# Optimization experiments

Measured on AMD Instinct MI355X. Metric: run time of the kernel, lower is better.

Reference implementation:

```python
import jax, jax.numpy as jnp
import numpy as np

B = 8192
DV, DT = 1024, 768          # visual / text dims
H = 256                     # hidden_dim
C = 5                       # num_classes
GH = 128                    # gate_hidden_dim
K = 8                       # graph_k
ALPHA = 0.5                 # graph_alpha
EW = 0.01                   # entropy_weight
FD = 2 * H                  # fused_dim = 512
GI = FD + C + H             # gate input dim = 773
NEG = -1.0e9
LN_EPS = 1e-5
BN_EPS = 1e-5
N_IMAGES = 512


def setup_inputs() -> dict:
    key = jax.random.key(0)
    ks = jax.random.split(key, 20)
    def rn(k, sh, s=0.02):
        return jax.random.normal(k, sh, dtype=jnp.float32) * s
    # x = [visual(1024) | text(768) | bbox_ctx(4) | img_uid(1)]
    xf = jax.random.normal(ks[0], (B, DV + DT), dtype=jnp.float32)
    bbox = jax.random.uniform(ks[1], (B, 4), dtype=jnp.float32)
    img = jax.random.randint(ks[2], (B, 1), 0, N_IMAGES).astype(jnp.float32)
    x = jnp.concatenate([xf, bbox, img], axis=1)  # [B, 1797]
    return {
        "x": x,
        "ln_v_g": jnp.ones((DV,), jnp.float32), "ln_v_b": jnp.zeros((DV,), jnp.float32),
        "ln_t_g": jnp.ones((DT,), jnp.float32), "ln_t_b": jnp.zeros((DT,), jnp.float32),
        "W_v": rn(ks[3], (DV, H)), "b_v": jnp.zeros((H,), jnp.float32),
        "W_t": rn(ks[4], (DT, H)), "b_t": jnp.zeros((H,), jnp.float32),
        "W_cp": rn(ks[5], (FD, C)), "b_cp": jnp.zeros((C,), jnp.float32),
        "W_ctx1": rn(ks[6], (FD, H)), "b_ctx1": jnp.zeros((H,), jnp.float32),
        "W_ctx2": rn(ks[7], (H, H)), "b_ctx2": jnp.zeros((H,), jnp.float32),
        "W_g1": rn(ks[8], (GI, GH)), "b_g1": jnp.zeros((GH,), jnp.float32),
        "W_g2": rn(ks[9], (GH, 2)), "b_g2": jnp.zeros((2,), jnp.float32),
        "W_gu1": rn(ks[10], (FD, FD)), "b_gu1": jnp.zeros((FD,), jnp.float32),
        "W_gu2": rn(ks[11], (FD, FD)), "b_gu2": jnp.zeros((FD,), jnp.float32),
        "W_c1": rn(ks[12], (FD, H)), "b_c1": jnp.zeros((H,), jnp.float32),
        "bn_g": jnp.ones((H,), jnp.float32), "bn_b": jnp.zeros((H,), jnp.float32),
        "W_c2": rn(ks[13], (H, C)), "b_c2": jnp.zeros((C,), jnp.float32),
    }


def _layernorm(x, g, b):
    m = jnp.mean(x, axis=-1, keepdims=True)
    v = jnp.mean((x - m) ** 2, axis=-1, keepdims=True)
    return (x - m) * jax.lax.rsqrt(v + LN_EPS) * g + b


def _knn_aggregate(features, coords, img):
    """KNN over 2D spatial coords with same-image masking; softmax-weighted gather."""
    n = features.shape[0]
    sq = jnp.sum(coords * coords, axis=1)
    d2 = sq[:, None] + sq[None, :] - 2.0 * (coords @ coords.T)
    sim = -jnp.sqrt(jnp.clip(d2, 0.0))                 # [B, B] = -cdist
    eye = jnp.eye(n, dtype=bool)
    same = (img[None, :] == img[:, None]) & ~eye
    has_neighbor = jnp.any(same, axis=1)
    sim_same = jnp.where(same, sim, NEG)
    sim = jnp.where(has_neighbor[:, None], sim_same, sim)
    sim = jnp.where(eye, NEG, sim)
    vals, idx = jax.lax.top_k(sim, K)                  # [B, K]
    w = jax.nn.softmax(vals, axis=1)
    return jnp.einsum('bk,bkd->bd', w, features[idx])  # gather + weighted sum


def reference(x, ln_v_g, ln_v_b, ln_t_g, ln_t_b, W_v, b_v, W_t, b_t,
              W_cp, b_cp, W_ctx1, b_ctx1, W_ctx2, b_ctx2,
              W_g1, b_g1, W_g2, b_g2, W_gu1, b_gu1, W_gu2, b_gu2,
              W_c1, b_c1, bn_g, bn_b, W_c2, b_c2):
    xv = x[:, 0:DV]
    xt = x[:, DV:DV + DT]
    coords = x[:, DV + DT:DV + DT + 2]     # bbox_ctx[:, :2]
    img = x[:, DV + DT + 4]                # img_uid[:, 0]

    fv = _layernorm(xv, ln_v_g, ln_v_b) @ W_v + b_v
    ft = _layernorm(xt, ln_t_g, ln_t_b) @ W_t + b_t
    base_fused = jnp.concatenate([fv, ft], axis=1)     # [B, FD]

    class_prior = jax.lax.stop_gradient(jax.nn.softmax(base_fused @ W_cp + b_cp, axis=1))

    neigh_agg = _knn_aggregate(base_fused, coords, img)
    spatial_token = jax.nn.relu(neigh_agg @ W_ctx1 + b_ctx1) @ W_ctx2 + b_ctx2
    spatial_token = jax.lax.stop_gradient(spatial_token)

    gate_in = jnp.concatenate([base_fused, class_prior, spatial_token], axis=1)
    gate_logits = jax.nn.relu(gate_in @ W_g1 + b_g1) @ W_g2 + b_g2
    gate_probs = jax.nn.softmax(gate_logits / 1.0, axis=1)  # temperature=1.0 (eval: dropout off)
    entropy = -jnp.sum(gate_probs * jnp.log(gate_probs + 1e-8), axis=1)
    entropy_loss = jnp.mean(entropy) * EW

    fused = jnp.concatenate([fv * gate_probs[:, 0:1], ft * gate_probs[:, 1:2]], axis=1)
    spatial_update = _knn_aggregate(fused, coords, img)
    upd = jax.nn.relu(spatial_update @ W_gu1 + b_gu1) @ W_gu2 + b_gu2
    fused = fused + ALPHA * upd

    h = fused @ W_c1 + b_c1
    # eval-mode BatchNorm1d: running_mean=0, running_var=1
    h = h * (bn_g / jnp.sqrt(1.0 + BN_EPS)) + bn_b
    h = jax.nn.relu(h)
    logits = h @ W_c2 + b_c2
    return logits, entropy_loss
```

## Files before the change

### kernel.cpp

```cpp
#include <hip/hip_runtime.h>
#include <math.h>

#define B_ROWS 8192
#define DV_DIM 1024
#define DT_DIM 768
#define H_DIM 256
#define C_CLS 5
#define GH_DIM 128
#define K_NN 8
#define FD_DIM 512
#define GIP_DIM 832
#define GI_REAL 773
#define XCOLS 1797
#define NEGV -1000000000.0f
#define LN_EPS_F 1e-5f
#define BN_EPS_F 1e-5f
#define N_IMG 512
#define EW_F 0.01f
#define ALPHA_F 0.5f

typedef __attribute__((ext_vector_type(8))) short short8v;
typedef __attribute__((ext_vector_type(4))) float f32x4;

__device__ inline short bf16r(float f) {
    unsigned u = __float_as_uint(f);
    return (short)((u + 0x7fffu + ((u >> 16) & 1u)) >> 16);
}

__device__ inline float bf2f(short s) {
    return __uint_as_float(((unsigned)(unsigned short)s) << 16);
}

struct PrepArgs {
    const float* W[8];
    short* h[8];
    int K[8];
    int N[8];
    int Kpad[8];
    int cnt[8];
};

__global__ void prep_all_kernel(PrepArgs a, const float* __restrict__ x,
                                float* __restrict__ cx, float* __restrict__ cy,
                                float* __restrict__ sq, int* __restrict__ imgi,
                                int* __restrict__ cnt) {
    int idx = blockIdx.x * blockDim.x + threadIdx.x;
#pragma unroll
    for (int s = 0; s < 8; ++s) {
        if (idx < a.cnt[s]) {
            int Kp = a.Kpad[s];
            int n = idx / Kp, k = idx - n * Kp;
            float f = (k < a.K[s]) ? a.W[s][(size_t)k * a.N[s] + n] : 0.f;
            a.h[s][idx] = bf16r(f);
            return;
        }
        idx -= a.cnt[s];
    }
    if (idx < B_ROWS) {
        const float* row = x + (size_t)idx * XCOLS;
        float av = row[DV_DIM + DT_DIM];
        float bv = row[DV_DIM + DT_DIM + 1];
        cx[idx] = av; cy[idx] = bv; sq[idx] = av * av + bv * bv;
        int m = (int)row[DV_DIM + DT_DIM + 4];
        imgi[idx] = m;
        atomicAdd(&cnt[m], 1);
    }
}

__global__ void scan_kernel(const int* __restrict__ cnt, int* __restrict__ start,
                            int* __restrict__ cursor) {
    __shared__ int s[N_IMG];
    int t = threadIdx.x;
    s[t] = cnt[t];
    __syncthreads();
    for (int off = 1; off < N_IMG; off <<= 1) {
        int v = (t >= off) ? s[t - off] : 0;
        __syncthreads();
        s[t] += v;
        __syncthreads();
    }
    int st = s[t] - cnt[t];
    start[t] = st;
    cursor[t] = st;
}

__global__ void scatter_kernel(const int* __restrict__ imgi, int* __restrict__ cursor,
                               int* __restrict__ perm) {
    int i = blockIdx.x * blockDim.x + threadIdx.x;
    if (i >= B_ROWS) return;
    int pos = atomicAdd(&cursor[imgi[i]], 1);
    perm[pos] = i;
}

#define KNN_BLOCKS 32
#define LN_BLOCKS (B_ROWS / 4)
__global__ __launch_bounds__(256) void lnknn_kernel(
    const float* __restrict__ x,
    const float* __restrict__ gv, const float* __restrict__ bv,
    const float* __restrict__ gt, const float* __restrict__ bt,
    short* __restrict__ xvh, short* __restrict__ xth,
    const float* __restrict__ cx, const float* __restrict__ cy,
    const float* __restrict__ sq, const int* __restrict__ imgi,
    const int* __restrict__ cnt, const int* __restrict__ start,
    const int* __restrict__ perm, int* __restrict__ knn_idx,
    float* __restrict__ knn_w) {
    if (blockIdx.x < KNN_BLOCKS) {
        int i = blockIdx.x * 256 + threadIdx.x;
        if (i >= B_ROWS) return;
        float xi = cx[i], yi = cy[i], si = sq[i];
        float vals[K_NN];
        int ids[K_NN];
#pragma unroll
        for (int k = 0; k < K_NN; ++k) { vals[k] = NEGV; ids[k] = i; }
        int m = imgi[i];
        int s = cnt[m];
        if (s >= 2) {
            int st = start[m];
            for (int t = 0; t < s; ++t) {
                int j = perm[st + t];
                if (j == i) continue;
                float d2 = si + sq[j] - 2.f * (xi * cx[j] + yi * cy[j]);
                d2 = fmaxf(d2, 0.f);
                float v = -sqrtf(d2);
                if (v > vals[K_NN - 1]) {
                    int p = K_NN - 1;
                    while (p > 0 && vals[p - 1] < v) {
                        vals[p] = vals[p - 1]; ids[p] = ids[p - 1]; --p;
                    }
                    vals[p] = v; ids[p] = j;
                }
            }
        } else {
            for (int j = 0; j < B_ROWS; ++j) {
                if (j == i) continue;
                float d2 = si + sq[j] - 2.f * (xi * cx[j] + yi * cy[j]);
                d2 = fmaxf(d2, 0.f);
                float v = -sqrtf(d2);
                if (v > vals[K_NN - 1]) {
                    int p = K_NN - 1;
                    while (p > 0 && vals[p - 1] < v) {
                        vals[p] = vals[p - 1]; ids[p] = ids[p - 1]; --p;
                    }
                    vals[p] = v; ids[p] = j;
                }
            }
        }
        float mx = vals[0];
        float e[K_NN];
        float sum = 0.f;
#pragma unroll
        for (int k = 0; k < K_NN; ++k) { e[k] = expf(vals[k] - mx); sum += e[k]; }
        float inv = 1.f / sum;
#pragma unroll
        for (int k = 0; k < K_NN; ++k) {
            knn_w[(size_t)i * K_NN + k] = e[k] * inv;
            knn_idx[(size_t)i * K_NN + k] = ids[k];
        }
        return;
    }
    int wave = threadIdx.x >> 6;
    int lane = threadIdx.x & 63;
    long row = (long)(blockIdx.x - KNN_BLOCKS) * 4 + wave;
    const float* xr = x + row * XCOLS;

    float v[16];
#pragma unroll
    for (int k = 0; k < 16; ++k) v[k] = xr[lane + 64 * k];
    float sum = 0.f;
#pragma unroll
    for (int k = 0; k < 16; ++k) sum += v[k];
#pragma unroll
    for (int off = 32; off; off >>= 1) sum += __shfl_xor(sum, off);
    float mean = sum * (1.f / DV_DIM);
    float vs = 0.f;
#pragma unroll
    for (int k = 0; k < 16; ++k) { float d = v[k] - mean; vs += d * d; }
#pragma unroll
    for (int off = 32; off; off >>= 1) vs += __shfl_xor(vs, off);
    float rs = rsqrtf(vs * (1.f / DV_DIM) + LN_EPS_F);
#pragma unroll
    for (int k = 0; k < 16; ++k) {
        int j = lane + 64 * k;
        float y = (v[k] - mean) * rs * gv[j] + bv[j];
        xvh[row * DV_DIM + j] = bf16r(y);
    }

    float u[12];
#pragma unroll
    for (int k = 0; k < 12; ++k) u[k] = xr[DV_DIM + lane + 64 * k];
    sum = 0.f;
#pragma unroll
    for (int k = 0; k < 12; ++k) sum += u[k];
#pragma unroll
    for (int off = 32; off; off >>= 1) sum += __shfl_xor(sum, off);
    mean = sum * (1.f / DT_DIM);
    vs = 0.f;
#pragma unroll
    for (int k = 0; k < 12; ++k) { float d = u[k] - mean; vs += d * d; }
#pragma unroll
    for (int off = 32; off; off >>= 1) vs += __shfl_xor(vs, off);
    rs = rsqrtf(vs * (1.f / DT_DIM) + LN_EPS_F);
#pragma unroll
    for (int k = 0; k < 12; ++k) {
        int j = lane + 64 * k;
        float y = (u[k] - mean) * rs * gt[j] + bt[j];
        xth[row * DT_DIM + j] = bf16r(y);
    }
}

__device__ inline int xcd_swz(int wg, int nwg) {
    int q = nwg >> 3, r = nwg & 7;
    int xc = wg & 7, ii = wg >> 3;
    return (xc < r ? xc * (q + 1) : r * (q + 1) + (xc - r) * q) + ii;
}

struct GemmPair {
    const short* Ah;
    const short* Bh;
    const float* bias;
    int K; int ncb; int colOff;
};

template <int MODE, int NF>
__global__ __launch_bounds__(256) void gemm2_kernel(
    GemmPair P0, GemmPair P1, int nblk0,
    short* __restrict__ Ch, int ldc,
    const short* __restrict__ auxh, const float* __restrict__ gpv) {
    constexpr int ASZ = 4096;
    constexpr int BSZ = 32 * NF * 64;
    __shared__ short lds[ASZ + BSZ];
    short* sAh = lds;
    short* sBh = lds + ASZ;

    const int tid = threadIdx.x;
    const int lane = tid & 63;
    const int wave = tid >> 6;
    const int wm = wave >> 1, wn = wave & 1;
    const int l15 = lane & 15, lq = lane >> 4;

    int wid = xcd_swz(blockIdx.x, gridDim.x);
    GemmPair G = P0;
    if (wid >= nblk0) { G = P1; wid -= nblk0; }

    const int panel = wid / G.ncb, cb = wid - panel * G.ncb;
    const long rowBase = (long)panel * 64;
    const int colBase = cb * (32 * NF);
    const int K = G.K;

    f32x4 acc[2][NF];
#pragma unroll
    for (int i = 0; i < 2; ++i)
#pragma unroll
        for (int j = 0; j < NF; ++j) acc[i][j] = (f32x4){0.f, 0.f, 0.f, 0.f};

    short8v pAh[2], pBh[NF];
    const int ar0 = tid >> 3, ac = tid & 7;
    const int ar1 = (tid + 256) >> 3;

    {
        long go0 = (rowBase + ar0) * K + ac * 8;
        long go1 = (rowBase + ar1) * K + ac * 8;
        pAh[0] = *(const short8v*)(G.Ah + go0);
        pAh[1] = *(const short8v*)(G.Ah + go1);
#pragma unroll
        for (int j = 0; j < NF; ++j) {
            int cid = tid + 256 * j;
            int cl = cid >> 3, c = cid & 7;
            long go = (colBase + cl) * (long)K + c * 8;
            pBh[j] = *(const short8v*)(G.Bh + go);
        }
    }

    const int nsteps = K >> 6;
    for (int s = 0; s < nsteps; ++s) {
        __syncthreads();
        {
            int off0 = ar0 * 64 + ((ac ^ (ar0 & 7)) << 3);
            int off1 = ar1 * 64 + ((ac ^ (ar1 & 7)) << 3);
            *(short8v*)(sAh + off0) = pAh[0];
            *(short8v*)(sAh + off1) = pAh[1];
#pragma unroll
            for (int j = 0; j < NF; ++j) {
                int cid = tid + 256 * j;
                int cl = cid >> 3, c = cid & 7;
                int off = cl * 64 + ((c ^ (cl & 7)) << 3);
                *(short8v*)(sBh + off) = pBh[j];
            }
        }
        __syncthreads();
        if (s + 1 < nsteps) {
            long ko = (long)(s + 1) * 64;
            long go0 = (rowBase + ar0) * K + ko + ac * 8;
            long go1 = (rowBase + ar1) * K + ko + ac * 8;
            pAh[0] = *(const short8v*)(G.Ah + go0);
            pAh[1] = *(const short8v*)(G.Ah + go1);
#pragma unroll
            for (int j = 0; j < NF; ++j) {
                int cid = tid + 256 * j;
                int cl = cid >> 3, c = cid & 7;
                long go = (colBase + cl) * (long)K + ko + c * 8;
                pBh[j] = *(const short8v*)(G.Bh + go);
            }
        }
#pragma unroll
        for (int ksub = 0; ksub < 2; ++ksub) {
            int cc = ksub * 4 + lq;
            short8v afh[2], bfh[NF];
#pragma unroll
            for (int mf = 0; mf < 2; ++mf) {
                int rr = wm * 32 + mf * 16 + l15;
                int off = rr * 64 + ((cc ^ (rr & 7)) << 3);
                afh[mf] = *(short8v*)(sAh + off);
            }
#pragma unroll
            for (int nf = 0; nf < NF; ++nf) {
                int cl = wn * (NF * 16) + nf * 16 + l15;
                int off = cl * 64 + ((cc ^ (cl & 7)) << 3);
                bfh[nf] = *(short8v*)(sBh + off);
            }
#pragma unroll
            for (int mf = 0; mf < 2; ++mf)
#pragma unroll
                for (int nf = 0; nf < NF; ++nf)
                    acc[mf][nf] = __builtin_amdgcn_mfma_f32_16x16x32_bf16(afh[mf], bfh[nf], acc[mf][nf], 0, 0, 0);
        }
    }

#pragma unroll
    for (int mf = 0; mf < 2; ++mf)
#pragma unroll
        for (int nf = 0; nf < NF; ++nf) {
            int col = colBase + wn * (NF * 16) + nf * 16 + l15;
            long row0 = rowBase + wm * 32 + mf * 16 + lq * 4;
#pragma unroll
            for (int rr = 0; rr < 4; ++rr) {
                long row = row0 + rr;
                float v = acc[mf][nf][rr] + G.bias[col];
                long o = row * ldc + G.colOff + col;
                if (MODE == 4) {
                    Ch[o] = bf16r(v);
                } else if (MODE == 3) {
                    Ch[o] = bf16r(fmaxf(v, 0.f));
                } else {
                    float g = gpv[row * 2 + (col >= H_DIM ? 1 : 0)];
                    float fv = bf2f(auxh[row * FD_DIM + col]) * g + ALPHA_F * v;
                    Ch[o] = bf16r(fv);
                }
            }
        }
}

__global__ __launch_bounds__(256) void post_base_kernel(
    const short* __restrict__ baseh, const float* __restrict__ Wcp,
    const float* __restrict__ bcp, const int* __restrict__ kidx,
    const float* __restrict__ wgt, short* __restrict__ gih,
    short* __restrict__ aggh) {
    int row = blockIdx.x;
    int t = threadIdx.x;
    short sa = baseh[(size_t)row * FD_DIM + t];
    short sb = baseh[(size_t)row * FD_DIM + t + 256];
    float a = bf2f(sa), b = bf2f(sb);

    __shared__ float red[C_CLS][256];
#pragma unroll
    for (int n = 0; n < C_CLS; ++n)
        red[n][t] = a * Wcp[t * C_CLS + n] + b * Wcp[(t + 256) * C_CLS + n];
    __syncthreads();
    for (int off = 128; off; off >>= 1) {
        if (t < off) {
#pragma unroll
            for (int n = 0; n < C_CLS; ++n) red[n][t] += red[n][t + off];
        }
        __syncthreads();
    }
    size_t go = (size_t)row * GIP_DIM;
    if (t == 0) {
        float lg[C_CLS];
#pragma unroll
        for (int n = 0; n < C_CLS; ++n) lg[n] = red[n][0] + bcp[n];
        float mx = lg[0];
#pragma unroll
        for (int n = 1; n < C_CLS; ++n) mx = fmaxf(mx, lg[n]);
        float s = 0.f;
        float e[C_CLS];
#pragma unroll
        for (int n = 0; n < C_CLS; ++n) { e[n] = expf(lg[n] - mx); s += e[n]; }
        float inv = 1.f / s;
#pragma unroll
        for (int n = 0; n < C_CLS; ++n) gih[go + FD_DIM + n] = bf16r(e[n] * inv);
    }
    gih[go + t] = sa;
    gih[go + t + 256] = sb;
    if (t < GIP_DIM - GI_REAL) gih[go + GI_REAL + t] = 0;

    int jj[K_NN];
    float ww[K_NN];
#pragma unroll
    for (int k = 0; k < K_NN; ++k) {
        jj[k] = kidx[(size_t)row * K_NN + k];
        ww[k] = wgt[(size_t)row * K_NN + k];
    }
#pragma unroll
    for (int half = 0; half < 2; ++half) {
        int d = t + half * 256;
        float s = 0.f;
#pragma unroll
        for (int k = 0; k < K_NN; ++k)
            s = fmaf(ww[k], bf2f(baseh[(size_t)jj[k] * FD_DIM + d]), s);
        aggh[(size_t)row * FD_DIM + d] = bf16r(s);
    }
}

__global__ __launch_bounds__(256) void gather_gate_kernel(
    const short* __restrict__ baseh, const int* __restrict__ kidx,
    const float* __restrict__ wgt, const float* __restrict__ gp,
    short* __restrict__ oh) {
    int row = blockIdx.x;
    int t = threadIdx.x;
    int jj[K_NN];
    float ww[K_NN], g0[K_NN], g1[K_NN];
#pragma unroll
    for (int k = 0; k < K_NN; ++k) {
        jj[k] = kidx[(size_t)row * K_NN + k];
        ww[k] = wgt[(size_t)row * K_NN + k];
        g0[k] = gp[(size_t)jj[k] * 2 + 0];
        g1[k] = gp[(size_t)jj[k] * 2 + 1];
    }
#pragma unroll
    for (int half = 0; half < 2; ++half) {
        int d = t + half * 256;
        float s = 0.f;
#pragma unroll
        for (int k = 0; k < K_NN; ++k) {
            float f = bf2f(baseh[(size_t)jj[k] * FD_DIM + d]);
            f *= (d < H_DIM) ? g0[k] : g1[k];
            s = fmaf(ww[k], f, s);
        }
        oh[(size_t)row * FD_DIM + d] = bf16r(s);
    }
}

__global__ __launch_bounds__(256) void ctxfused_kernel(
    const short* __restrict__ aggh, const short* __restrict__ wx1, const float* __restrict__ b1,
    const short* __restrict__ wx2, const float* __restrict__ b2, short* __restrict__ gih) {
    __shared__ short lds[2048 + 16384 + 8192];
    short* sA = lds;
    short* sB = lds + 2048;
    short* sH = lds + 2048 + 16384;

    const int tid = threadIdx.x;
    const int lane = tid & 63;
    const int wave = tid >> 6;
    const int l15 = lane & 15, lq = lane >> 4;
    int panel = xcd_swz(blockIdx.x, gridDim.x);
    const long rowBase = (long)panel * 32;

    const int ar = tid >> 3, ac = tid & 7;

    f32x4 acc[2][4];
#pragma unroll
    for (int i = 0; i < 2; ++i)
#pragma unroll
        for (int j = 0; j < 4; ++j) acc[i][j] = (f32x4){0.f, 0.f, 0.f, 0.f};

    short8v pA, pB[8];
    {
        pA = *(const short8v*)(aggh + (rowBase + ar) * 512 + ac * 8);
#pragma unroll
        for (int j = 0; j < 8; ++j) {
            int cid = tid + 256 * j;
            int cl = cid >> 3, c = cid & 7;
            pB[j] = *(const short8v*)(wx1 + (long)cl * 512 + c * 8);
        }
    }
    for (int s = 0; s < 8; ++s) {
        __syncthreads();
        *(short8v*)(sA + ar * 64 + ((ac ^ (ar & 7)) << 3)) = pA;
#pragma unroll
        for (int j = 0; j < 8; ++j) {
            int cid = tid + 256 * j;
            int cl = cid >> 3, c = cid & 7;
            *(short8v*)(sB + cl * 64 + ((c ^ (cl & 7)) << 3)) = pB[j];
        }
        __syncthreads();
        if (s + 1 < 8) {
            long ko = (long)(s + 1) * 64;
            pA = *(const short8v*)(aggh + (rowBase + ar) * 512 + ko + ac * 8);
#pragma unroll
            for (int j = 0; j < 8; ++j) {
                int cid = tid + 256 * j;
                int cl = cid >> 3, c = cid & 7;
                pB[j] = *(const short8v*)(wx1 + (long)cl * 512 + ko + c * 8);
            }
        }
#pragma unroll
        for (int ksub = 0; ksub < 2; ++ksub) {
            int cc = ksub * 4 + lq;
            short8v af[2], bf[4];
#pragma unroll
            for (int mf = 0; mf < 2; ++mf) {
                int rr = mf * 16 + l15;
                af[mf] = *(short8v*)(sA + rr * 64 + ((cc ^ (rr & 7)) << 3));
            }
#pragma unroll
            for (int nf = 0; nf < 4; ++nf) {
                int cl = wave * 64 + nf * 16 + l15;
                bf[nf] = *(short8v*)(sB + cl * 64 + ((cc ^ (cl & 7)) << 3));
            }
#pragma unroll
            for (int mf = 0; mf < 2; ++mf)
#pragma unroll
                for (int nf = 0; nf < 4; ++nf)
                    acc[mf][nf] = __builtin_amdgcn_mfma_f32_16x16x32_bf16(af[mf], bf[nf], acc[mf][nf], 0, 0, 0);
        }
    }
    __syncthreads();
#pragma unroll
    for (int mf = 0; mf < 2; ++mf)
#pragma unroll
        for (int nf = 0; nf < 4; ++nf) {
            int col = wave * 64 + nf * 16 + l15;
            int sub = col >> 6, cch = (col >> 3) & 7, ce = col & 7;
#pragma unroll
            for (int rr = 0; rr < 4; ++rr) {
                int r = mf * 16 + lq * 4 + rr;
                float v = fmaxf(acc[mf][nf][rr] + b1[col], 0.f);
                sH[sub * 2048 + r * 64 + ((cch ^ (r & 7)) << 3) + ce] = bf16r(v);
            }
        }
    f32x4 acc2[2][4];
#pragma unroll
    for (int i = 0; i < 2; ++i)
#pragma unroll
        for (int j = 0; j < 4; ++j) acc2[i][j] = (f32x4){0.f, 0.f, 0.f, 0.f};
    for (int s = 0; s < 4; ++s) {
        __syncthreads();
#pragma unroll
        for (int j = 0; j < 8; ++j) {
            int cid = tid + 256 * j;
            int cl = cid >> 3, c = cid & 7;
            short8v b = *(const short8v*)(wx2 + (long)cl * 256 + s * 64 + c * 8);
            *(short8v*)(sB + cl * 64 + ((c ^ (cl & 7)) << 3)) = b;
        }
        __syncthreads();
#pragma unroll
        for (int ksub = 0; ksub < 2; ++ksub) {
            int cc = ksub * 4 + lq;
            short8v af[2], bf[4];
#pragma unroll
            for (int mf = 0; mf < 2; ++mf) {
                int rr = mf * 16 + l15;
                af[mf] = *(short8v*)(sH + s * 2048 + rr * 64 + ((cc ^ (rr & 7)) << 3));
            }
#pragma unroll
            for (int nf = 0; nf < 4; ++nf) {
                int cl = wave * 64 + nf * 16 + l15;
                bf[nf] = *(short8v*)(sB + cl * 64 + ((cc ^ (cl & 7)) << 3));
            }
#pragma unroll
            for (int mf = 0; mf < 2; ++mf)
#pragma unroll
                for (int nf = 0; nf < 4; ++nf)
                    acc2[mf][nf] = __builtin_amdgcn_mfma_f32_16x16x32_bf16(af[mf], bf[nf], acc2[mf][nf], 0, 0, 0);
        }
    }
#pragma unroll
    for (int mf = 0; mf < 2; ++mf)
#pragma unroll
        for (int nf = 0; nf < 4; ++nf) {
            int col = wave * 64 + nf * 16 + l15;
#pragma unroll
            for (int rr = 0; rr < 4; ++rr) {
                long row = rowBase + mf * 16 + lq * 4 + rr;
                gih[row * GIP_DIM + FD_DIM + C_CLS + col] = bf16r(acc2[mf][nf][rr] + b2[col]);
            }
        }
}

__global__ __launch_bounds__(256) void g1gate_kernel(
    const short* __restrict__ gih, const short* __restrict__ wg1, const float* __restrict__ b1,
    const float* __restrict__ W2, const float* __restrict__ b2,
    float* __restrict__ gp, float* __restrict__ entpart) {
    __shared__ float hls[64 * 128];
    short* sA = (short*)hls;
    short* sB = sA + 4096;
    __shared__ float entrow[64];

    const int tid = threadIdx.x;
    const int lane = tid & 63;
    const int wave = tid >> 6;
    const int wm = wave >> 1, wn = wave & 1;
    const int l15 = lane & 15, lq = lane >> 4;
    int panel = xcd_swz(blockIdx.x, gridDim.x);
    const long rowBase = (long)panel * 64;

    const int ar0 = tid >> 3, ac = tid & 7;
    const int ar1 = (tid + 256) >> 3;
    constexpr int K = GIP_DIM;

    f32x4 acc[2][4];
#pragma unroll
    for (int i = 0; i < 2; ++i)
#pragma unroll
        for (int j = 0; j < 4; ++j) acc[i][j] = (f32x4){0.f, 0.f, 0.f, 0.f};

    short8v pA0, pA1, pB[4];
    {
        pA0 = *(const short8v*)(gih + (rowBase + ar0) * K + ac * 8);
        pA1 = *(const short8v*)(gih + (rowBase + ar1) * K + ac * 8);
#pragma unroll
        for (int j = 0; j < 4; ++j) {
            int cid = tid + 256 * j;
            int cl = cid >> 3, c = cid & 7;
            pB[j] = *(const short8v*)(wg1 + (long)cl * K + c * 8);
        }
    }
    const int nsteps = K >> 6;
    for (int s = 0; s < nsteps; ++s) {
        __syncthreads();
        *(short8v*)(sA + ar0 * 64 + ((ac ^ (ar0 & 7)) << 3)) = pA0;
        *(short8v*)(sA + ar1 * 64 + ((ac ^ (ar1 & 7)) << 3)) = pA1;
#pragma unroll
        for (int j = 0; j < 4; ++j) {
            int cid = tid + 256 * j;
            int cl = cid >> 3, c = cid & 7;
            *(short8v*)(sB + cl * 64 + ((c ^ (cl & 7)) << 3)) = pB[j];
        }
        __syncthreads();
        if (s + 1 < nsteps) {
            long ko = (long)(s + 1) * 64;
            pA0 = *(const short8v*)(gih + (rowBase + ar0) * K + ko + ac * 8);
            pA1 = *(const short8v*)(gih + (rowBase + ar1) * K + ko + ac * 8);
#pragma unroll
            for (int j = 0; j < 4; ++j) {
                int cid = tid + 256 * j;
                int cl = cid >> 3, c = cid & 7;
                pB[j] = *(const short8v*)(wg1 + (long)cl * K + ko + c * 8);
            }
        }
#pragma unroll
        for (int ksub = 0; ksub < 2; ++ksub) {
            int cc = ksub * 4 + lq;
            short8v af[2], bf[4];
#pragma unroll
            for (int mf = 0; mf < 2; ++mf) {
                int rr = wm * 32 + mf * 16 + l15;
                af[mf] = *(short8v*)(sA + rr * 64 + ((cc ^ (rr & 7)) << 3));
            }
#pragma unroll
            for (int nf = 0; nf < 4; ++nf) {
                int cl = wn * 64 + nf * 16 + l15;
                bf[nf] = *(short8v*)(sB + cl * 64 + ((cc ^ (cl & 7)) << 3));
            }
#pragma unroll
            for (int mf = 0; mf < 2; ++mf)
#pragma unroll
                for (int nf = 0; nf < 4; ++nf)
                    acc[mf][nf] = __builtin_amdgcn_mfma_f32_16x16x32_bf16(af[mf], bf[nf], acc[mf][nf], 0, 0, 0);
        }
    }
    __syncthreads();
#pragma unroll
    for (int mf = 0; mf < 2; ++mf)
#pragma unroll
        for (int nf = 0; nf < 4; ++nf) {
            int col = wn * 64 + nf * 16 + l15;
#pragma unroll
            for (int rr = 0; rr < 4; ++rr) {
                int r = wm * 32 + mf * 16 + lq * 4 + rr;
                hls[r * 128 + col] = fmaxf(acc[mf][nf][rr] + b1[col], 0.f);
            }
        }
    __syncthreads();
    {
        int r = tid >> 2, p = tid & 3;
        float a0 = 0.f, a1 = 0.f;
#pragma unroll
        for (int i = 0; i < 32; ++i) {
            int c = p + i * 4;
            float hv = hls[r * 128 + c];
            a0 = fmaf(hv, W2[c * 2 + 0], a0);
            a1 = fmaf(hv, W2[c * 2 + 1], a1);
        }
        a0 += __shfl_xor(a0, 1); a1 += __shfl_xor(a1, 1);
        a0 += __shfl_xor(a0, 2); a1 += __shfl_xor(a1, 2);
        if (p == 0) {
            float l0 = a0 + b2[0], l1 = a1 + b2[1];
            float mx = fmaxf(l0, l1);
            float e0 = expf(l0 - mx), e1 = expf(l1 - mx);
            float ssum = e0 + e1;
            float p0 = e0 / ssum, p1 = e1 / ssum;
            long grow = rowBase + r;
            gp[grow * 2 + 0] = p0;
            gp[grow * 2 + 1] = p1;
            entrow[r] = -(p0 * logf(p0 + 1e-8f) + p1 * logf(p1 + 1e-8f));
        }
    }
    __syncthreads();
    if (tid == 0) {
        float s = 0.f;
        for (int r = 0; r < 64; ++r) s += entrow[r];
        entpart[blockIdx.x] = s;
    }
}

__global__ __launch_bounds__(256) void c1logits_kernel(
    const short* __restrict__ fusedh, const short* __restrict__ wc1, const float* __restrict__ b1,
    const float* __restrict__ bng, const float* __restrict__ bnb,
    const float* __restrict__ W2, const float* __restrict__ b2,
    const float* __restrict__ entpart, float* __restrict__ out) {
    __shared__ short lds[2048 + 16384];
    short* sA = lds;
    short* sB = lds + 2048;
    float* hls = (float*)lds;

    const int tid = threadIdx.x;
    const int lane = tid & 63;
    const int wave = tid >> 6;
    const int l15 = lane & 15, lq = lane >> 4;
    int panel = xcd_swz(blockIdx.x, gridDim.x);
    const long rowBase = (long)panel * 32;
    const int ar = tid >> 3, ac = tid & 7;

    f32x4 acc[2][4];
#pragma unroll
    for (int i = 0; i < 2; ++i)
#pragma unroll
        for (int j = 0; j < 4; ++j) acc[i][j] = (f32x4){0.f, 0.f, 0.f, 0.f};

    short8v pA, pB[8];
    {
        pA = *(const short8v*)(fusedh + (rowBase + ar) * 512 + ac * 8);
#pragma unroll
        for (int j = 0; j < 8; ++j) {
            int cid = tid + 256 * j;
            int cl = cid >> 3, c = cid & 7;
            pB[j] = *(const short8v*)(wc1 + (long)cl * 512 + c * 8);
        }
    }
    for (int s = 0; s < 8; ++s) {
        __syncthreads();
        *(short8v*)(sA + ar * 64 + ((ac ^ (ar & 7)) << 3)) = pA;
#pragma unroll
        for (int j = 0; j < 8; ++j) {
            int cid = tid + 256 * j;
            int cl = cid >> 3, c = cid & 7;
            *(short8v*)(sB + cl * 64 + ((c ^ (cl & 7)) << 3)) = pB[j];
        }
        __syncthreads();
        if (s + 1 < 8) {
            long ko = (long)(s + 1) * 64;
            pA = *(const short8v*)(fusedh + (rowBase + ar) * 512 + ko + ac * 8);
#pragma unroll
            for (int j = 0; j < 8; ++j) {
                int cid = tid + 256 * j;
                int cl = cid >> 3, c = cid & 7;
                pB[j] = *(const short8v*)(wc1 + (long)cl * 512 + ko + c * 8);
            }
        }
#pragma unroll
        for (int ksub = 0; ksub < 2; ++ksub) {
            int cc = ksub * 4 + lq;
            short8v af[2], bf[4];
#pragma unroll
            for (int mf = 0; mf < 2; ++mf) {
                int rr = mf * 16 + l15;
                af[mf] = *(short8v*)(sA + rr * 64 + ((cc ^ (rr & 7)) << 3));
            }
#pragma unroll
            for (int nf = 0; nf < 4; ++nf) {
                int cl = wave * 64 + nf * 16 + l15;
                bf[nf] = *(short8v*)(sB + cl * 64 + ((cc ^ (cl & 7)) << 3));
            }
#pragma unroll
            for (int mf = 0; mf < 2; ++mf)
#pragma unroll
                for (int nf = 0; nf < 4; ++nf)
                    acc[mf][nf] = __builtin_amdgcn_mfma_f32_16x16x32_bf16(af[mf], bf[nf], acc[mf][nf], 0, 0, 0);
        }
    }
    __syncthreads();
#pragma unroll
    for (int mf = 0; mf < 2; ++mf)
#pragma unroll
        for (int nf = 0; nf < 4; ++nf) {
            int col = wave * 64 + nf * 16 + l15;
            float scale = bng[col] * rsqrtf(1.f + BN_EPS_F);
            float shift = bnb[col];
#pragma unroll
            for (int rr = 0; rr < 4; ++rr) {
                int r = mf * 16 + lq * 4 + rr;
                float v = (acc[mf][nf][rr] + b1[col]) * scale + shift;
                hls[r * 256 + col] = fmaxf(v, 0.f);
            }
        }
    __syncthreads();
    {
        int r = tid >> 3, p = tid & 7;
        float a[C_CLS];
#pragma unroll
        for (int n = 0; n < C_CLS; ++n) a[n] = 0.f;
#pragma unroll
        for (int i = 0; i < 32; ++i) {
            int c = p + i * 8;
            float hv = hls[r * 256 + c];
#pragma unroll
            for (int n = 0; n < C_CLS; ++n) a[n] = fmaf(hv, W2[c * 5 + n], a[n]);
        }
#pragma unroll
        for (int n = 0; n < C_CLS; ++n) {
            a[n] += __shfl_xor(a[n], 1);
            a[n] += __shfl_xor(a[n], 2);
            a[n] += __shfl_xor(a[n], 4);
        }
        if (p == 0) {
            long grow = rowBase + r;
#pragma unroll
            for (int n = 0; n < C_CLS; ++n) out[grow * C_CLS + n] = a[n] + b2[n];
        }
    }
    if (blockIdx.x == 0 && tid < 64) {
        float s = entpart[tid] + entpart[tid + 64];
        for (int off = 32; off; off >>= 1) s += __shfl_down(s, off);
        if (tid == 0) out[(size_t)B_ROWS * C_CLS] = s * (EW_F / (float)B_ROWS);
    }
}

extern "C" void kernel_launch(void* const* d_in, const int* in_sizes, int n_in,
                              void* d_out, int out_size, void* d_ws, size_t ws_size,
                              hipStream_t stream) {
    const float* x = (const float*)d_in[0];
    const float* ln_v_g = (const float*)d_in[1];
    const float* ln_v_b = (const float*)d_in[2];
    const float* ln_t_g = (const float*)d_in[3];
    const float* ln_t_b = (const float*)d_in[4];
    const float* W_v = (const float*)d_in[5];
    const float* b_v = (const float*)d_in[6];
    const float* W_t = (const float*)d_in[7];
    const float* b_t = (const float*)d_in[8];
    const float* W_cp = (const float*)d_in[9];
    const float* b_cp = (const float*)d_in[10];
    const float* W_ctx1 = (const float*)d_in[11];
    const float* b_ctx1 = (const float*)d_in[12];
    const float* W_ctx2 = (const float*)d_in[13];
    const float* b_ctx2 = (const float*)d_in[14];
    const float* W_g1 = (const float*)d_in[15];
    const float* b_g1 = (const float*)d_in[16];
    const float* W_g2 = (const float*)d_in[17];
    const float* b_g2 = (const float*)d_in[18];
    const float* W_gu1 = (const float*)d_in[19];
    const float* b_gu1 = (const float*)d_in[20];
    const float* W_gu2 = (const float*)d_in[21];
    const float* b_gu2 = (const float*)d_in[22];
    const float* W_c1 = (const float*)d_in[23];
    const float* b_c1 = (const float*)d_in[24];
    const float* bn_g = (const float*)d_in[25];
    const float* bn_b = (const float*)d_in[26];
    const float* W_c2 = (const float*)d_in[27];
    const float* b_c2 = (const float*)d_in[28];

    float* out = (float*)d_out;

    char* wsb = (char*)d_ws;
    size_t off = 0;
    auto alloc = [&](size_t bytes) {
        char* p = wsb + off;
        off += (bytes + 255) & ~(size_t)255;
        return p;
    };
    short* baseh = (short*)alloc((size_t)B_ROWS * FD_DIM * 2);
    short* aggh = (short*)alloc((size_t)B_ROWS * FD_DIM * 2);
    float* gp = (float*)alloc((size_t)B_ROWS * 2 * 4);
    float* entpart = (float*)alloc(128 * 4);
    float* cxv = (float*)alloc((size_t)B_ROWS * 4);
    float* cyv = (float*)alloc((size_t)B_ROWS * 4);
    float* sqv = (float*)alloc((size_t)B_ROWS * 4);
    float* wgt = (float*)alloc((size_t)B_ROWS * K_NN * 4);
    int* imgi = (int*)alloc((size_t)B_ROWS * 4);
    int* cnt = (int*)alloc(N_IMG * 4);
    int* startb = (int*)alloc(N_IMG * 4);
    int* cursor = (int*)alloc(N_IMG * 4);
    int* perm = (int*)alloc((size_t)B_ROWS * 4);
    int* kidx = (int*)alloc((size_t)B_ROWS * K_NN * 4);
    short* wv_h = (short*)alloc(256 * 1024 * 2);
    short* wt_h = (short*)alloc(256 * 768 * 2);
    short* wx1_h = (short*)alloc(256 * 512 * 2);
    short* wx2_h = (short*)alloc(256 * 256 * 2);
    short* wg1_h = (short*)alloc(128 * GIP_DIM * 2);
    short* wu1_h = (short*)alloc(512 * 512 * 2);
    short* wu2_h = (short*)alloc(512 * 512 * 2);
    short* wc1_h = (short*)alloc(256 * 512 * 2);
    char* R = alloc((size_t)B_ROWS * (DV_DIM + DT_DIM) * 2);
    short* xvh = (short*)R;
    short* xth = xvh + (size_t)B_ROWS * DV_DIM;
    short* gih = (short*)R;
    short* guh = gih + (size_t)B_ROWS * GIP_DIM;
    short* fusedh = aggh;

    dim3 blk(256);
    dim3 gridRows((B_ROWS + 255) / 256);

    PrepArgs pa;
    const float* pw[8] = {W_v, W_t, W_ctx1, W_ctx2, W_g1, W_gu1, W_gu2, W_c1};
    short* ph[8] = {wv_h, wt_h, wx1_h, wx2_h, wg1_h, wu1_h, wu2_h, wc1_h};
    int pK[8] = {1024, 768, 512, 256, GI_REAL, 512, 512, 512};
    int pN[8] = {256, 256, 256, 256, 128, 512, 512, 256};
    int pKp[8] = {1024, 768, 512, 256, GIP_DIM, 512, 512, 512};
    int total = 0;
    for (int s = 0; s < 8; ++s) {
        pa.W[s] = pw[s]; pa.h[s] = ph[s];
        pa.K[s] = pK[s]; pa.N[s] = pN[s]; pa.Kpad[s] = pKp[s];
        pa.cnt[s] = pN[s] * pKp[s];
        total += pa.cnt[s];
    }
    hipMemsetAsync(cnt, 0, N_IMG * sizeof(int), stream);
    prep_all_kernel<<<(total + B_ROWS + 255) / 256, blk, 0, stream>>>(
        pa, x, cxv, cyv, sqv, imgi, cnt);

    scan_kernel<<<1, N_IMG, 0, stream>>>(cnt, startb, cursor);
    scatter_kernel<<<gridRows, blk, 0, stream>>>(imgi, cursor, perm);

    lnknn_kernel<<<KNN_BLOCKS + LN_BLOCKS, blk, 0, stream>>>(
        x, ln_v_g, ln_v_b, ln_t_g, ln_t_b, xvh, xth,
        cxv, cyv, sqv, imgi, cnt, startb, perm, kidx, wgt);

    GemmPair fvP{xvh, wv_h, b_v, 1024, 4, 0};
    GemmPair ftP{xth, wt_h, b_t, 768, 4, 256};
    gemm2_kernel<4, 2><<<1024, blk, 0, stream>>>(fvP, ftP, 512, baseh, FD_DIM,
                                                 nullptr, nullptr);

    post_base_kernel<<<B_ROWS, blk, 0, stream>>>(baseh, W_cp, b_cp, kidx, wgt, gih, aggh);

    ctxfused_kernel<<<256, blk, 0, stream>>>(aggh, wx1_h, b_ctx1, wx2_h, b_ctx2, gih);

    g1gate_kernel<<<128, blk, 0, stream>>>(gih, wg1_h, b_g1, W_g2, b_g2, gp, entpart);

    gather_gate_kernel<<<B_ROWS, blk, 0, stream>>>(baseh, kidx, wgt, gp, aggh);
    GemmPair u1P{aggh, wu1_h, b_gu1, 512, 4, 0};
    gemm2_kernel<3, 4><<<512, blk, 0, stream>>>(u1P, u1P, 512, guh, FD_DIM,
                                                nullptr, nullptr);
    GemmPair u2P{guh, wu2_h, b_gu2, 512, 4, 0};
    gemm2_kernel<5, 4><<<512, blk, 0, stream>>>(u2P, u2P, 512, fusedh, FD_DIM,
                                                baseh, gp);

    c1logits_kernel<<<256, blk, 0, stream>>>(fusedh, wc1_h, b_c1, bn_g, bn_b,
                                             W_c2, b_c2, entpart, out);

    (void)in_sizes; (void)n_in; (void)out_size; (void)ws_size;
}
```

Before: 177.2 us.

## Fuse the two update-MLP GEMMs into one kernel and vectorize LayerNorm IO

Replaces the two separate gemm2 launches for the gated-update MLP (ReLU(agg@Wgu1)@Wgu2 plus residual blend) with one kernel. Each block handles a 16-row panel and keeps the ReLU hidden activations in LDS, so the guh intermediate never makes a round trip through global memory and one launch is saved. In exchange, every small-panel block streams both full 512x512 weight matrices, which adds a lot of L2 traffic, and uses about 50KB of LDS, which limits occupancy. The LayerNorm part now uses 16-byte vectorized loads and 8-byte vectorized bf16 stores.

```diff
diff --git a/kernel.cpp b/kernel.cpp
--- a/kernel.cpp
+++ b/kernel.cpp
@@ -20,7 +20,9 @@
 #define ALPHA_F 0.5f
 
 typedef __attribute__((ext_vector_type(8))) short short8v;
+typedef __attribute__((ext_vector_type(4))) short short4v;
 typedef __attribute__((ext_vector_type(4))) float f32x4;
+typedef __attribute__((ext_vector_type(4))) float float4v;
 
 __device__ inline short bf16r(float f) {
     unsigned u = __float_as_uint(f);
@@ -165,7 +167,8 @@
 
     float v[16];
 #pragma unroll
-    for (int k = 0; k < 16; ++k) v[k] = xr[lane + 64 * k];
+    for (int k = 0; k < 4; ++k)
+        __builtin_memcpy(&v[k * 4], xr + lane * 4 + 256 * k, 16);
     float sum = 0.f;
 #pragma unroll
     for (int k = 0; k < 16; ++k) sum += v[k];
@@ -179,15 +182,21 @@
     for (int off = 32; off; off >>= 1) vs += __shfl_xor(vs, off);
     float rs = rsqrtf(vs * (1.f / DV_DIM) + LN_EPS_F);
 #pragma unroll
-    for (int k = 0; k < 16; ++k) {
-        int j = lane + 64 * k;
-        float y = (v[k] - mean) * rs * gv[j] + bv[j];
-        xvh[row * DV_DIM + j] = bf16r(y);
+    for (int k = 0; k < 4; ++k) {
+        int j0 = lane * 4 + 256 * k;
+        float4v g4 = *(const float4v*)(gv + j0);
+        float4v b4 = *(const float4v*)(bv + j0);
+        short4v o;
+#pragma unroll
+        for (int j = 0; j < 4; ++j)
+            o[j] = bf16r((v[k * 4 + j] - mean) * rs * g4[j] + b4[j]);
+        *(short4v*)(xvh + row * DV_DIM + j0) = o;
     }
 
     float u[12];
 #pragma unroll
-    for (int k = 0; k < 12; ++k) u[k] = xr[DV_DIM + lane + 64 * k];
+    for (int k = 0; k < 3; ++k)
+        __builtin_memcpy(&u[k * 4], xr + DV_DIM + lane * 4 + 256 * k, 16);
     sum = 0.f;
 #pragma unroll
     for (int k = 0; k < 12; ++k) sum += u[k];
@@ -201,10 +210,15 @@
     for (int off = 32; off; off >>= 1) vs += __shfl_xor(vs, off);
     rs = rsqrtf(vs * (1.f / DT_DIM) + LN_EPS_F);
 #pragma unroll
-    for (int k = 0; k < 12; ++k) {
-        int j = lane + 64 * k;
-        float y = (u[k] - mean) * rs * gt[j] + bt[j];
-        xth[row * DT_DIM + j] = bf16r(y);
+    for (int k = 0; k < 3; ++k) {
+        int j0 = lane * 4 + 256 * k;
+        float4v g4 = *(const float4v*)(gt + j0);
+        float4v b4 = *(const float4v*)(bt + j0);
+        short4v o;
+#pragma unroll
+        for (int j = 0; j < 4; ++j)
+            o[j] = bf16r((u[k * 4 + j] - mean) * rs * g4[j] + b4[j]);
+        *(short4v*)(xth + row * DT_DIM + j0) = o;
     }
 }
 
@@ -224,8 +238,7 @@
 template <int MODE, int NF>
 __global__ __launch_bounds__(256) void gemm2_kernel(
     GemmPair P0, GemmPair P1, int nblk0,
-    short* __restrict__ Ch, int ldc,
-    const short* __restrict__ auxh, const float* __restrict__ gpv) {
+    short* __restrict__ Ch, int ldc) {
     constexpr int ASZ = 4096;
     constexpr int BSZ = 32 * NF * 64;
     __shared__ short lds[ASZ + BSZ];
@@ -336,16 +349,7 @@
             for (int rr = 0; rr < 4; ++rr) {
                 long row = row0 + rr;
                 float v = acc[mf][nf][rr] + G.bias[col];
-                long o = row * ldc + G.colOff + col;
-                if (MODE == 4) {
-                    Ch[o] = bf16r(v);
-                } else if (MODE == 3) {
-                    Ch[o] = bf16r(fmaxf(v, 0.f));
-                } else {
-                    float g = gpv[row * 2 + (col >= H_DIM ? 1 : 0)];
-                    float fv = bf2f(auxh[row * FD_DIM + col]) * g + ALPHA_F * v;
-                    Ch[o] = bf16r(fv);
-                }
+                Ch[row * ldc + G.colOff + col] = bf16r(v);
             }
         }
 }
@@ -575,6 +579,109 @@
                 gih[row * GIP_DIM + FD_DIM + C_CLS + col] = bf16r(acc2[mf][nf][rr] + b2[col]);
             }
         }
+}
+
+__global__ __launch_bounds__(256) void ufused_kernel(
+    const short* __restrict__ aggh, const short* __restrict__ wu1, const float* __restrict__ b1,
+    const short* __restrict__ wu2, const float* __restrict__ b2,
+    const short* __restrict__ baseh, const float* __restrict__ gp,
+    short* __restrict__ fusedh) {
+    __shared__ short sA[1024];
+    __shared__ short sB[16384];
+    __shared__ short sH[8192];
+
+    const int tid = threadIdx.x;
+    const int lane = tid & 63;
+    const int wave = tid >> 6;
+    const int l15 = lane & 15, lq = lane >> 4;
+    int panel = xcd_swz(blockIdx.x, gridDim.x);
+    const long rowBase = (long)panel * 16;
+
+#pragma unroll 1
+    for (int nh = 0; nh < 2; ++nh) {
+        f32x4 acc[4];
+#pragma unroll
+        for (int j = 0; j < 4; ++j) acc[j] = (f32x4){0.f, 0.f, 0.f, 0.f};
+#pragma unroll 1
+        for (int s = 0; s < 8; ++s) {
+            __syncthreads();
+            if (tid < 128) {
+                int ar = tid >> 3, c = tid & 7;
+                short8v a = *(const short8v*)(aggh + (rowBase + ar) * 512 + s * 64 + c * 8);
+                *(short8v*)(sA + ar * 64 + ((c ^ (ar & 7)) << 3)) = a;
+            }
+#pragma unroll
+            for (int j = 0; j < 8; ++j) {
+                int cid = tid + 256 * j;
+                int cl = cid >> 3, c = cid & 7;
+                short8v b = *(const short8v*)(wu1 + (long)(nh * 256 + cl) * 512 + s * 64 + c * 8);
+                *(short8v*)(sB + cl * 64 + ((c ^ (cl & 7)) << 3)) = b;
+            }
+            __syncthreads();
+#pragma unroll
+            for (int ksub = 0; ksub < 2; ++ksub) {
+                int cc = ksub * 4 + lq;
+                short8v af = *(short8v*)(sA + l15 * 64 + ((cc ^ (l15 & 7)) << 3));
+#pragma unroll
+                for (int nf = 0; nf < 4; ++nf) {
+                    int cl = wave * 64 + nf * 16 + l15;
+                    short8v bf = *(short8v*)(sB + cl * 64 + ((cc ^ (cl & 7)) << 3));
+                    acc[nf] = __builtin_amdgcn_mfma_f32_16x16x32_bf16(af, bf, acc[nf], 0, 0, 0);
+                }
+            }
+        }
+#pragma unroll
+        for (int nf = 0; nf < 4; ++nf) {
+            int col = nh * 256 + wave * 64 + nf * 16 + l15;
+            int sub = col >> 6, cch = (col >> 3) & 7, ce = col & 7;
+#pragma unroll
+            for (int rr = 0; rr < 4; ++rr) {
+                int r = lq * 4 + rr;
+                float v = fmaxf(acc[nf][rr] + b1[col], 0.f);
+                sH[sub * 1024 + r * 64 + ((cch ^ (r & 7)) << 3) + ce] = bf16r(v);
+            }
+        }
+    }
+#pragma unroll 1
+    for (int nh = 0; nh < 2; ++nh) {
+        f32x4 acc[4];
+#pragma unroll
+        for (int j = 0; j < 4; ++j) acc[j] = (f32x4){0.f, 0.f, 0.f, 0.f};
+#pragma unroll 1
+        for (int s = 0; s < 8; ++s) {
+            __syncthreads();
+#pragma unroll
+            for (int j = 0; j < 8; ++j) {
+                int cid = tid + 256 * j;
+                int cl = cid >> 3, c = cid & 7;
+                short8v b = *(const short8v*)(wu2 + (long)(nh * 256 + cl) * 512 + s * 64 + c * 8);
+                *(short8v*)(sB + cl * 64 + ((c ^ (cl & 7)) << 3)) = b;
+            }
+            __syncthreads();
+#pragma unroll
+            for (int ksub = 0; ksub < 2; ++ksub) {
+                int cc = ksub * 4 + lq;
+                short8v af = *(short8v*)(sH + s * 1024 + l15 * 64 + ((cc ^ (l15 & 7)) << 3));
+#pragma unroll
+                for (int nf = 0; nf < 4; ++nf) {
+                    int cl = wave * 64 + nf * 16 + l15;
+                    short8v bf = *(short8v*)(sB + cl * 64 + ((cc ^ (cl & 7)) << 3));
+                    acc[nf] = __builtin_amdgcn_mfma_f32_16x16x32_bf16(af, bf, acc[nf], 0, 0, 0);
+                }
+            }
+        }
+#pragma unroll
+        for (int nf = 0; nf < 4; ++nf) {
+            int col = nh * 256 + wave * 64 + nf * 16 + l15;
+#pragma unroll
+            for (int rr = 0; rr < 4; ++rr) {
+                long row = rowBase + lq * 4 + rr;
+                float g = gp[row * 2 + (col >= H_DIM ? 1 : 0)];
+                float fv = bf2f(baseh[row * FD_DIM + col]) * g + ALPHA_F * (acc[nf][rr] + b2[col]);
+                fusedh[row * FD_DIM + col] = bf16r(fv);
+            }
+        }
+    }
 }
 
 __global__ __launch_bounds__(256) void g1gate_kernel(
@@ -894,7 +1001,6 @@
     short* xvh = (short*)R;
     short* xth = xvh + (size_t)B_ROWS * DV_DIM;
     short* gih = (short*)R;
-    short* guh = gih + (size_t)B_ROWS * GIP_DIM;
     short* fusedh = aggh;
 
     dim3 blk(256);
@@ -926,8 +1032,7 @@
 
     GemmPair fvP{xvh, wv_h, b_v, 1024, 4, 0};
     GemmPair ftP{xth, wt_h, b_t, 768, 4, 256};
-    gemm2_kernel<4, 2><<<1024, blk, 0, stream>>>(fvP, ftP, 512, baseh, FD_DIM,
-                                                 nullptr, nullptr);
+    gemm2_kernel<4, 2><<<1024, blk, 0, stream>>>(fvP, ftP, 512, baseh, FD_DIM);
 
     post_base_kernel<<<B_ROWS, blk, 0, stream>>>(baseh, W_cp, b_cp, kidx, wgt, gih, aggh);
 
@@ -936,12 +1041,8 @@
     g1gate_kernel<<<128, blk, 0, stream>>>(gih, wg1_h, b_g1, W_g2, b_g2, gp, entpart);
 
     gather_gate_kernel<<<B_ROWS, blk, 0, stream>>>(baseh, kidx, wgt, gp, aggh);
-    GemmPair u1P{aggh, wu1_h, b_gu1, 512, 4, 0};
-    gemm2_kernel<3, 4><<<512, blk, 0, stream>>>(u1P, u1P, 512, guh, FD_DIM,
-                                                nullptr, nullptr);
-    GemmPair u2P{guh, wu2_h, b_gu2, 512, 4, 0};
-    gemm2_kernel<5, 4><<<512, blk, 0, stream>>>(u2P, u2P, 512, fusedh, FD_DIM,
-                                                baseh, gp);
+    ufused_kernel<<<512, blk, 0, stream>>>(aggh, wu1_h, b_gu1, wu2_h, b_gu2,
+                                           baseh, gp, fusedh);
 
     c1logits_kernel<<<256, blk, 0, stream>>>(fusedh, wc1_h, b_c1, bn_g, bn_b,
                                              W_c2, b_c2, entpart, out);
```

New measurement: 191.6 us. 1.08x slower.

## Fuse LayerNorm into the visual/text projection GEMM prologue

Applied to the files above, without the earlier changes.

Replaces the separate LayerNorm kernel and the bf16 normalized-activation buffers with a single kernel that computes per-row mean/rstd for each 64-row panel, then normalizes fp32 x on the fly while staging A tiles into LDS for the MFMA GEMM. This removes a launch and the write/read of the normalized bf16 intermediates. Each column block re-reads the raw fp32 rows for both statistics and tiles, increasing global reads of x, and variance uses a single-pass E[x^2]-mean^2 formula. Workspace buffers for gate input and update are given their own allocations instead of aliasing the removed region.

```diff
diff --git a/kernel.cpp b/kernel.cpp
--- a/kernel.cpp
+++ b/kernel.cpp
@@ -92,20 +92,35 @@
     perm[pos] = i;
 }
 
+__device__ inline int xcd_swz(int wg, int nwg) {
+    int q = nwg >> 3, r = nwg & 7;
+    int xc = wg & 7, ii = wg >> 3;
+    return (xc < r ? xc * (q + 1) : r * (q + 1) + (xc - r) * q) + ii;
+}
+
+struct LnSeg {
+    int xOff;
+    int K;
+    const float* gamma;
+    const float* beta;
+    const short* Bh;
+    const float* bias;
+    int colOff;
+};
+
 #define KNN_BLOCKS 32
-#define LN_BLOCKS (B_ROWS / 4)
-__global__ __launch_bounds__(256) void lnknn_kernel(
-    const float* __restrict__ x,
-    const float* __restrict__ gv, const float* __restrict__ bv,
-    const float* __restrict__ gt, const float* __restrict__ bt,
-    short* __restrict__ xvh, short* __restrict__ xth,
+#define FVFT_BLOCKS 1024
+
+__global__ __launch_bounds__(256) void lnfvft_kernel(
+    const float* __restrict__ x, LnSeg S0, LnSeg S1, short* __restrict__ baseh,
     const float* __restrict__ cx, const float* __restrict__ cy,
     const float* __restrict__ sq, const int* __restrict__ imgi,
     const int* __restrict__ cnt, const int* __restrict__ start,
     const int* __restrict__ perm, int* __restrict__ knn_idx,
     float* __restrict__ knn_w) {
+    const int tid = threadIdx.x;
     if (blockIdx.x < KNN_BLOCKS) {
-        int i = blockIdx.x * 256 + threadIdx.x;
+        int i = blockIdx.x * 256 + tid;
         if (i >= B_ROWS) return;
         float xi = cx[i], yi = cy[i], si = sq[i];
         float vals[K_NN];
@@ -158,60 +173,142 @@
         }
         return;
     }
-    int wave = threadIdx.x >> 6;
-    int lane = threadIdx.x & 63;
-    long row = (long)(blockIdx.x - KNN_BLOCKS) * 4 + wave;
-    const float* xr = x + row * XCOLS;
-
-    float v[16];
-#pragma unroll
-    for (int k = 0; k < 16; ++k) v[k] = xr[lane + 64 * k];
-    float sum = 0.f;
-#pragma unroll
-    for (int k = 0; k < 16; ++k) sum += v[k];
-#pragma unroll
-    for (int off = 32; off; off >>= 1) sum += __shfl_xor(sum, off);
-    float mean = sum * (1.f / DV_DIM);
-    float vs = 0.f;
-#pragma unroll
-    for (int k = 0; k < 16; ++k) { float d = v[k] - mean; vs += d * d; }
-#pragma unroll
-    for (int off = 32; off; off >>= 1) vs += __shfl_xor(vs, off);
-    float rs = rsqrtf(vs * (1.f / DV_DIM) + LN_EPS_F);
-#pragma unroll
-    for (int k = 0; k < 16; ++k) {
-        int j = lane + 64 * k;
-        float y = (v[k] - mean) * rs * gv[j] + bv[j];
-        xvh[row * DV_DIM + j] = bf16r(y);
-    }
-
-    float u[12];
-#pragma unroll
-    for (int k = 0; k < 12; ++k) u[k] = xr[DV_DIM + lane + 64 * k];
-    sum = 0.f;
-#pragma unroll
-    for (int k = 0; k < 12; ++k) sum += u[k];
-#pragma unroll
-    for (int off = 32; off; off >>= 1) sum += __shfl_xor(sum, off);
-    mean = sum * (1.f / DT_DIM);
-    vs = 0.f;
-#pragma unroll
-    for (int k = 0; k < 12; ++k) { float d = u[k] - mean; vs += d * d; }
-#pragma unroll
-    for (int off = 32; off; off >>= 1) vs += __shfl_xor(vs, off);
-    rs = rsqrtf(vs * (1.f / DT_DIM) + LN_EPS_F);
-#pragma unroll
-    for (int k = 0; k < 12; ++k) {
-        int j = lane + 64 * k;
-        float y = (u[k] - mean) * rs * gt[j] + bt[j];
-        xth[row * DT_DIM + j] = bf16r(y);
-    }
-}
-
-__device__ inline int xcd_swz(int wg, int nwg) {
-    int q = nwg >> 3, r = nwg & 7;
-    int xc = wg & 7, ii = wg >> 3;
-    return (xc < r ? xc * (q + 1) : r * (q + 1) + (xc - r) * q) + ii;
+
+    __shared__ float smean[64];
+    __shared__ float srstd[64];
+    __shared__ short lds[4096 + 4096];
+    short* sAh = lds;
+    short* sBh = lds + 4096;
+
+    const int lane = tid & 63;
+    const int wave = tid >> 6;
+    const int wm = wave >> 1, wn = wave & 1;
+    const int l15 = lane & 15, lq = lane >> 4;
+
+    int wid = xcd_swz(blockIdx.x - KNN_BLOCKS, FVFT_BLOCKS);
+    LnSeg S = S0;
+    if (wid >= 512) { S = S1; wid -= 512; }
+    const int panel = wid >> 2, cb = wid & 3;
+    const long rowBase = (long)panel * 64;
+    const int colBase = cb * 64;
+    const int K = S.K;
+
+    {
+        int r = tid >> 2, p = tid & 3;
+        const float* xr = x + (rowBase + r) * (long)XCOLS + S.xOff;
+        float sum = 0.f, ss = 0.f;
+        int nq = K >> 2;
+        for (int c = p; c < nq; c += 4) {
+            float t4[4];
+            __builtin_memcpy(t4, xr + c * 4, 16);
+#pragma unroll
+            for (int j = 0; j < 4; ++j) { sum += t4[j]; ss += t4[j] * t4[j]; }
+        }
+        sum += __shfl_xor(sum, 1);
+        sum += __shfl_xor(sum, 2);
+        ss += __shfl_xor(ss, 1);
+        ss += __shfl_xor(ss, 2);
+        if (p == 0) {
+            float mean = sum / (float)K;
+            float var = fmaxf(ss / (float)K - mean * mean, 0.f);
+            smean[r] = mean;
+            srstd[r] = rsqrtf(var + LN_EPS_F);
+        }
+    }
+    __syncthreads();
+
+    f32x4 acc[2][2];
+#pragma unroll
+    for (int i = 0; i < 2; ++i)
+#pragma unroll
+        for (int j = 0; j < 2; ++j) acc[i][j] = (f32x4){0.f, 0.f, 0.f, 0.f};
+
+    const int ar0 = tid >> 3, ac = tid & 7;
+    const int ar1 = ar0 + 32;
+
+    float pAf[2][8];
+    short8v pBh[2];
+    {
+        __builtin_memcpy(pAf[0], x + (rowBase + ar0) * (long)XCOLS + S.xOff + ac * 8, 32);
+        __builtin_memcpy(pAf[1], x + (rowBase + ar1) * (long)XCOLS + S.xOff + ac * 8, 32);
+#pragma unroll
+        for (int j = 0; j < 2; ++j) {
+            int cid = tid + 256 * j;
+            int cl = cid >> 3, c = cid & 7;
+            pBh[j] = *(const short8v*)(S.Bh + (colBase + cl) * (long)K + c * 8);
+        }
+    }
+
+    const int nsteps = K >> 6;
+    for (int s = 0; s < nsteps; ++s) {
+        __syncthreads();
+        {
+#pragma unroll
+            for (int h = 0; h < 2; ++h) {
+                int ar = h ? ar1 : ar0;
+                float m = smean[ar], rsd = srstd[ar];
+                short8v o;
+#pragma unroll
+                for (int j = 0; j < 8; ++j) {
+                    int col = s * 64 + ac * 8 + j;
+                    o[j] = bf16r((pAf[h][j] - m) * rsd * S.gamma[col] + S.beta[col]);
+                }
+                *(short8v*)(sAh + ar * 64 + ((ac ^ (ar & 7)) << 3)) = o;
+            }
+#pragma unroll
+            for (int j = 0; j < 2; ++j) {
+                int cid = tid + 256 * j;
+                int cl = cid >> 3, c = cid & 7;
+                *(short8v*)(sBh + cl * 64 + ((c ^ (cl & 7)) << 3)) = pBh[j];
+            }
+        }
+        __syncthreads();
+        if (s + 1 < nsteps) {
+            long ko = (long)(s + 1) * 64;
+            __builtin_memcpy(pAf[0], x + (rowBase + ar0) * (long)XCOLS + S.xOff + ko + ac * 8, 32);
+            __builtin_memcpy(pAf[1], x + (rowBase + ar1) * (long)XCOLS + S.xOff + ko + ac * 8, 32);
+#pragma unroll
+            for (int j = 0; j < 2; ++j) {
+                int cid = tid + 256 * j;
+                int cl = cid >> 3, c = cid & 7;
+                pBh[j] = *(const short8v*)(S.Bh + (colBase + cl) * (long)K + ko + c * 8);
+            }
+        }
+#pragma unroll
+        for (int ksub = 0; ksub < 2; ++ksub) {
+            int cc = ksub * 4 + lq;
+            short8v afh[2], bfh[2];
+#pragma unroll
+            for (int mf = 0; mf < 2; ++mf) {
+                int rr = wm * 32 + mf * 16 + l15;
+                afh[mf] = *(short8v*)(sAh + rr * 64 + ((cc ^ (rr & 7)) << 3));
+            }
+#pragma unroll
+            for (int nf = 0; nf < 2; ++nf) {
+                int cl = wn * 32 + nf * 16 + l15;
+                bfh[nf] = *(short8v*)(sBh + cl * 64 + ((cc ^ (cl & 7)) << 3));
+            }
+#pragma unroll
+            for (int mf = 0; mf < 2; ++mf)
+#pragma unroll
+                for (int nf = 0; nf < 2; ++nf)
+                    acc[mf][nf] = __builtin_amdgcn_mfma_f32_16x16x32_bf16(afh[mf], bfh[nf], acc[mf][nf], 0, 0, 0);
+        }
+    }
+
+#pragma unroll
+    for (int mf = 0; mf < 2; ++mf)
+#pragma unroll
+        for (int nf = 0; nf < 2; ++nf) {
+            int col = colBase + wn * 32 + nf * 16 + l15;
+            long row0 = rowBase + wm * 32 + mf * 16 + lq * 4;
+#pragma unroll
+            for (int rr = 0; rr < 4; ++rr) {
+                long row = row0 + rr;
+                float v = acc[mf][nf][rr] + S.bias[col];
+                baseh[row * FD_DIM + S.colOff + col] = bf16r(v);
+            }
+        }
 }
 
 struct GemmPair {
@@ -337,9 +434,7 @@
                 long row = row0 + rr;
                 float v = acc[mf][nf][rr] + G.bias[col];
                 long o = row * ldc + G.colOff + col;
-                if (MODE == 4) {
-                    Ch[o] = bf16r(v);
-                } else if (MODE == 3) {
+                if (MODE == 3) {
                     Ch[o] = bf16r(fmaxf(v, 0.f));
                 } else {
                     float g = gpv[row * 2 + (col >= H_DIM ? 1 : 0)];
@@ -870,6 +965,8 @@
     };
     short* baseh = (short*)alloc((size_t)B_ROWS * FD_DIM * 2);
     short* aggh = (short*)alloc((size_t)B_ROWS * FD_DIM * 2);
+    short* guh = (short*)alloc((size_t)B_ROWS * FD_DIM * 2);
+    short* gih = (short*)alloc((size_t)B_ROWS * GIP_DIM * 2);
     float* gp = (float*)alloc((size_t)B_ROWS * 2 * 4);
     float* entpart = (float*)alloc(128 * 4);
     float* cxv = (float*)alloc((size_t)B_ROWS * 4);
@@ -890,11 +987,6 @@
     short* wu1_h = (short*)alloc(512 * 512 * 2);
     short* wu2_h = (short*)alloc(512 * 512 * 2);
     short* wc1_h = (short*)alloc(256 * 512 * 2);
-    char* R = alloc((size_t)B_ROWS * (DV_DIM + DT_DIM) * 2);
-    short* xvh = (short*)R;
-    short* xth = xvh + (size_t)B_ROWS * DV_DIM;
-    short* gih = (short*)R;
-    short* guh = gih + (size_t)B_ROWS * GIP_DIM;
     short* fusedh = aggh;
 
     dim3 blk(256);
@@ -920,14 +1012,10 @@
     scan_kernel<<<1, N_IMG, 0, stream>>>(cnt, startb, cursor);
     scatter_kernel<<<gridRows, blk, 0, stream>>>(imgi, cursor, perm);
 
-    lnknn_kernel<<<KNN_BLOCKS + LN_BLOCKS, blk, 0, stream>>>(
-        x, ln_v_g, ln_v_b, ln_t_g, ln_t_b, xvh, xth,
-        cxv, cyv, sqv, imgi, cnt, startb, perm, kidx, wgt);
-
-    GemmPair fvP{xvh, wv_h, b_v, 1024, 4, 0};
-    GemmPair ftP{xth, wt_h, b_t, 768, 4, 256};
-    gemm2_kernel<4, 2><<<1024, blk, 0, stream>>>(fvP, ftP, 512, baseh, FD_DIM,
-                                                 nullptr, nullptr);
+    LnSeg S0{0, DV_DIM, ln_v_g, ln_v_b, wv_h, b_v, 0};
+    LnSeg S1{DV_DIM, DT_DIM, ln_t_g, ln_t_b, wt_h, b_t, 256};
+    lnfvft_kernel<<<KNN_BLOCKS + FVFT_BLOCKS, blk, 0, stream>>>(
+        x, S0, S1, baseh, cxv, cyv, sqv, imgi, cnt, startb, perm, kidx, wgt);
 
     post_base_kernel<<<B_ROWS, blk, 0, stream>>>(baseh, W_cp, b_cp, kidx, wgt, gih, aggh);
 
```

Measured after the change: 192.0 us. +8.4%, slower.
